# Performance work log

Hardware: AMD Instinct MI355X
Metric: run time of the kernel (lower is better)

The kernel has to match this reference:

```python
import jax, jax.numpy as jnp
import numpy as np

WS = 7          # window_size
NH = 4          # num_heads
C = 128         # channels
N = WS * WS     # tokens per window = 49
BW = 4096       # number of windows total (batch * windows_per_image)
NW = 64         # windows per image (mask leading dim)


def _rel_pos_index(ws):
    coords = np.stack(np.meshgrid(np.arange(ws), np.arange(ws), indexing='ij'))
    cf = coords.reshape(2, -1)
    rel = (cf[:, :, None] - cf[:, None, :]).transpose(1, 2, 0)
    rel[:, :, 0] += ws - 1
    rel[:, :, 1] += ws - 1
    rel[:, :, 0] *= 2 * ws - 1
    return jnp.asarray(rel.sum(-1).ravel(), dtype=jnp.int32)  # [N*N]


def setup_inputs() -> dict:
    key = jax.random.key(0)
    ks = jax.random.split(key, 6)
    x = jax.random.normal(ks[0], (BW, N, C), dtype=jnp.float32)
    qkv_w = jax.random.normal(ks[1], (C, 3 * C), dtype=jnp.float32) * 0.02
    qkv_b = jnp.zeros((3 * C,), dtype=jnp.float32)
    proj_w = jax.random.normal(ks[2], (C, C), dtype=jnp.float32) * 0.02
    proj_b = jnp.zeros((C,), dtype=jnp.float32)
    bias_table = jax.random.normal(ks[3], ((2 * WS - 1) ** 2, NH), dtype=jnp.float32) * 0.02
    # Swin shifted-window mask: 0 where attention allowed, -100 where blocked
    keep = jax.random.bernoulli(ks[4], 0.5, (NW, N, N))
    mask = jnp.where(keep, 0.0, -100.0).astype(jnp.float32)
    return {"x": x, "qkv_w": qkv_w, "qkv_b": qkv_b, "proj_w": proj_w,
            "proj_b": proj_b, "bias_table": bias_table, "mask": mask}


def reference(x, qkv_w, qkv_b, proj_w, proj_b, bias_table, mask):
    B_, n, c = x.shape
    h = NH
    d = c // h
    scale = d ** -0.5

    qkv = x @ qkv_w + qkv_b                       # [B_, N, 3C]
    qkv = qkv.reshape(B_, n, 3, h, d).transpose(2, 0, 3, 1, 4)  # [3, B_, h, N, d]
    q, k, v = qkv[0], qkv[1], qkv[2]

    attn = jnp.einsum('bhnd,bhmd->bhnm', q * scale, k)          # [B_, h, N, N]

    idx = _rel_pos_index(WS)
    rpb = bias_table[idx].reshape(n, n, h).transpose(2, 0, 1)   # [h, N, N]
    attn = attn + rpb[None]

    nW = mask.shape[0]
    attn = attn.reshape(-1, nW, h, n, n) + mask[None, :, None]  # [B, nW, h, N, N]
    attn = attn.reshape(-1, h, n, n)
    attn = jax.nn.softmax(attn, axis=-1)

    out = jnp.einsum('bhnm,bhmd->bhnd', attn, v)  # [B_, h, N, d]
    out = out.transpose(0, 2, 1, 3).reshape(B_, n, c)
    return out @ proj_w + proj_b
```

## Files before the change

### kernel.cpp

```cpp
#include <hip/hip_runtime.h>

#define NTOK 49
#define CH   128
#define NHEAD 4
#define SCALE 0.17677669529663687f

typedef __bf16 bf16x8 __attribute__((ext_vector_type(8)));
typedef short  s16x8  __attribute__((ext_vector_type(8)));
typedef float  f32x4  __attribute__((ext_vector_type(4)));

__device__ __forceinline__ unsigned short f2bf(float f) {
  unsigned int u = __builtin_bit_cast(unsigned int, f);
  u += 0x7FFFu + ((u >> 16) & 1u);
  return (unsigned short)(u >> 16);
}

__device__ __forceinline__ f32x4 mfma_bf16(s16x8 a, s16x8 b, f32x4 c) {
  return __builtin_amdgcn_mfma_f32_16x16x32_bf16(
      __builtin_bit_cast(bf16x8, a), __builtin_bit_cast(bf16x8, b), c, 0, 0, 0);
}

__global__ void prep_kernel(const float* __restrict__ qkv_w,
                            const float* __restrict__ proj_w,
                            const float* __restrict__ bias_table,
                            unsigned short* __restrict__ wT,
                            unsigned short* __restrict__ pT,
                            float* __restrict__ rpb) {
  int t = blockIdx.x * 256 + threadIdx.x;
  if (t < 384 * 128) {
    int n = t >> 7, k = t & 127;
    float v = qkv_w[k * 384 + n];
    if (n < 128) v *= SCALE;
    wT[n * 128 + k] = f2bf(v);
  } else if (t < 384 * 128 + 128 * 128) {
    int u = t - 384 * 128;
    int n = u >> 7, k = u & 127;
    pT[n * 128 + k] = f2bf(proj_w[k * 128 + n]);
  } else if (t < 384 * 128 + 128 * 128 + NHEAD * NTOK * NTOK) {
    int u = t - (384 * 128 + 128 * 128);
    int h = u / (NTOK * NTOK);
    int ij = u % (NTOK * NTOK);
    int i = ij / NTOK, j = ij % NTOK;
    int idx = (i / 7 - j / 7 + 6) * 13 + (i % 7 - j % 7 + 6);
    rpb[h * (NTOK * NTOK) + ij] = bias_table[idx * NHEAD + h];
  }
}

__global__ __launch_bounds__(256, 2)
void attn_fused_kernel(const float* __restrict__ x,
                       const float* __restrict__ qkv_b,
                       const float* __restrict__ proj_b,
                       const float* __restrict__ mask,
                       const unsigned short* __restrict__ wT,
                       const unsigned short* __restrict__ pT,
                       const float* __restrict__ rpb,
                       float* __restrict__ out) {
  __shared__ __align__(16) char smem_raw[76800];
  unsigned short* const Xs     = (unsigned short*)smem_raw;
  unsigned short* const QKbase = (unsigned short*)(smem_raw + 17408);
  unsigned short* const VTbase = (unsigned short*)(smem_raw + 58368);

  const int w    = blockIdx.x;
  const int tid  = threadIdx.x;
  const int wave = tid >> 6;
  const int lane = tid & 63;
  const int quad = lane >> 4;
  const int l16  = lane & 15;
  const int h    = wave;

  unsigned short* const qs = QKbase + wave * 5120;
  unsigned short* const ks = qs + 2560;
  unsigned short* const ps = QKbase + wave * 5120;
  unsigned short* const vt = VTbase + wave * 2304;

  const f32x4 fzero = {0.f, 0.f, 0.f, 0.f};

  {
    const float* xw = x + (size_t)w * (NTOK * CH);
    for (int t = tid; t < NTOK * 32; t += 256) {
      const int row = t >> 5;
      const int c4  = (t & 31) << 2;
      const float4 v = *(const float4*)(xw + row * CH + c4);
      ushort4 pk;
      pk.x = f2bf(v.x); pk.y = f2bf(v.y); pk.z = f2bf(v.z); pk.w = f2bf(v.w);
      *(ushort4*)(Xs + row * 136 + c4) = pk;
    }
    for (int t = tid; t < 15 * 32; t += 256) {
      const int row = 49 + (t >> 5);
      const int c4  = (t & 31) << 2;
      ushort4 z; z.x = 0; z.y = 0; z.z = 0; z.w = 0;
      *(ushort4*)(Xs + row * 136 + c4) = z;
    }
  }
  __syncthreads();

#pragma unroll
  for (int part = 0; part < 3; ++part) {
    f32x4 acc[4][2];
#pragma unroll
    for (int mt = 0; mt < 4; ++mt)
#pragma unroll
      for (int nt = 0; nt < 2; ++nt) acc[mt][nt] = fzero;
    const int nbase = part * 128 + h * 32;
#pragma unroll
    for (int kt = 0; kt < 4; ++kt) {
      s16x8 a[4], b[2];
#pragma unroll
      for (int mt = 0; mt < 4; ++mt)
        a[mt] = *(const s16x8*)(Xs + (mt * 16 + l16) * 136 + kt * 32 + quad * 8);
#pragma unroll
      for (int nt = 0; nt < 2; ++nt)
        b[nt] = *(const s16x8*)(wT + (size_t)(nbase + nt * 16 + l16) * 128 + kt * 32 + quad * 8);
#pragma unroll
      for (int mt = 0; mt < 4; ++mt)
#pragma unroll
        for (int nt = 0; nt < 2; ++nt)
          acc[mt][nt] = mfma_bf16(a[mt], b[nt], acc[mt][nt]);
    }
#pragma unroll
    for (int nt = 0; nt < 2; ++nt) {
      float bias = qkv_b[nbase + nt * 16 + l16];
      if (part == 0) bias *= SCALE;
#pragma unroll
      for (int mt = 0; mt < 4; ++mt)
#pragma unroll
        for (int r = 0; r < 4; ++r) {
          const int row = mt * 16 + quad * 4 + r;
          const int col = nt * 16 + l16;
          const unsigned short bv = f2bf(acc[mt][nt][r] + bias);
          if (part == 0)      qs[row * 40 + col] = bv;
          else if (part == 1) ks[row * 40 + col] = bv;
          else                vt[col * 72 + row] = bv;
        }
    }
  }
  __syncthreads();

  s16x8 qf[4], kf[4];
#pragma unroll
  for (int mt = 0; mt < 4; ++mt)
    qf[mt] = *(const s16x8*)(qs + (mt * 16 + l16) * 40 + quad * 8);
#pragma unroll
  for (int nt = 0; nt < 4; ++nt)
    kf[nt] = *(const s16x8*)(ks + (nt * 16 + l16) * 40 + quad * 8);
  f32x4 s[4][4];
#pragma unroll
  for (int mt = 0; mt < 4; ++mt)
#pragma unroll
    for (int nt = 0; nt < 4; ++nt)
      s[mt][nt] = mfma_bf16(qf[mt], kf[nt], fzero);

  const float* maskw = mask + (size_t)(w & 63) * (NTOK * NTOK);
  const float* rpbh  = rpb + h * (NTOK * NTOK);
  float rinv[4][4];
#pragma unroll
  for (int mt = 0; mt < 4; ++mt) {
#pragma unroll
    for (int r = 0; r < 4; ++r) {
      const int i = mt * 16 + quad * 4 + r;
      float vals[4];
      float vmax = -1e30f;
#pragma unroll
      for (int nt = 0; nt < 4; ++nt) {
        const int j = nt * 16 + l16;
        float v = -1e30f;
        if (i < NTOK && j < NTOK) {
          const int ij = i * NTOK + j;
          v = s[mt][nt][r] + rpbh[ij] + maskw[ij];
        }
        vals[nt] = v;
        vmax = fmaxf(vmax, v);
      }
#pragma unroll
      for (int off = 1; off < 16; off <<= 1)
        vmax = fmaxf(vmax, __shfl_xor(vmax, off, 64));
      float rsum = 0.f;
#pragma unroll
      for (int nt = 0; nt < 4; ++nt) {
        const float e = __expf(vals[nt] - vmax);
        vals[nt] = e;
        rsum += e;
      }
#pragma unroll
      for (int off = 1; off < 16; off <<= 1)
        rsum += __shfl_xor(rsum, off, 64);
      rinv[mt][r] = 1.f / rsum;
#pragma unroll
      for (int nt = 0; nt < 4; ++nt)
        ps[i * 72 + nt * 16 + l16] = f2bf(vals[nt]);
    }
  }

  f32x4 o[4][2];
#pragma unroll
  for (int mt = 0; mt < 4; ++mt)
#pragma unroll
    for (int nt = 0; nt < 2; ++nt) o[mt][nt] = fzero;
#pragma unroll
  for (int kt = 0; kt < 2; ++kt) {
    s16x8 pf[4], vf[2];
#pragma unroll
    for (int mt = 0; mt < 4; ++mt)
      pf[mt] = *(const s16x8*)(ps + (mt * 16 + l16) * 72 + kt * 32 + quad * 8);
#pragma unroll
    for (int nt = 0; nt < 2; ++nt)
      vf[nt] = *(const s16x8*)(vt + (nt * 16 + l16) * 72 + kt * 32 + quad * 8);
#pragma unroll
    for (int mt = 0; mt < 4; ++mt)
#pragma unroll
      for (int nt = 0; nt < 2; ++nt)
        o[mt][nt] = mfma_bf16(pf[mt], vf[nt], o[mt][nt]);
  }

  unsigned short* const ao = Xs;
#pragma unroll
  for (int mt = 0; mt < 4; ++mt)
#pragma unroll
    for (int nt = 0; nt < 2; ++nt)
#pragma unroll
      for (int r = 0; r < 4; ++r) {
        const int row = mt * 16 + quad * 4 + r;
        const int col = h * 32 + nt * 16 + l16;
        ao[row * 136 + col] = f2bf(o[mt][nt][r] * rinv[mt][r]);
      }
  __syncthreads();

  f32x4 po[4][2];
#pragma unroll
  for (int mt = 0; mt < 4; ++mt)
#pragma unroll
    for (int nt = 0; nt < 2; ++nt) po[mt][nt] = fzero;
#pragma unroll
  for (int kt = 0; kt < 4; ++kt) {
    s16x8 a[4], b[2];
#pragma unroll
    for (int mt = 0; mt < 4; ++mt)
      a[mt] = *(const s16x8*)(ao + (mt * 16 + l16) * 136 + kt * 32 + quad * 8);
#pragma unroll
    for (int nt = 0; nt < 2; ++nt)
      b[nt] = *(const s16x8*)(pT + (size_t)(h * 32 + nt * 16 + l16) * 128 + kt * 32 + quad * 8);
#pragma unroll
    for (int mt = 0; mt < 4; ++mt)
#pragma unroll
      for (int nt = 0; nt < 2; ++nt)
        po[mt][nt] = mfma_bf16(a[mt], b[nt], po[mt][nt]);
  }
  float* outw = out + (size_t)w * (NTOK * CH);
#pragma unroll
  for (int nt = 0; nt < 2; ++nt) {
    const int col = h * 32 + nt * 16 + l16;
    const float pb = proj_b[col];
#pragma unroll
    for (int mt = 0; mt < 4; ++mt)
#pragma unroll
      for (int r = 0; r < 4; ++r) {
        const int row = mt * 16 + quad * 4 + r;
        if (row < NTOK) outw[row * CH + col] = po[mt][nt][r] + pb;
      }
  }
}

extern "C" void kernel_launch(void* const* d_in, const int* in_sizes, int n_in,
                              void* d_out, int out_size, void* d_ws, size_t ws_size,
                              hipStream_t stream) {
  (void)in_sizes; (void)n_in; (void)out_size; (void)ws_size;
  const float* x          = (const float*)d_in[0];
  const float* qkv_w      = (const float*)d_in[1];
  const float* qkv_b      = (const float*)d_in[2];
  const float* proj_w     = (const float*)d_in[3];
  const float* proj_b     = (const float*)d_in[4];
  const float* bias_table = (const float*)d_in[5];
  const float* mask       = (const float*)d_in[6];
  float* out = (float*)d_out;

  unsigned short* wT = (unsigned short*)d_ws;
  unsigned short* pT = wT + 384 * 128;
  float* rpb = (float*)(pT + 128 * 128);

  const int prep_items = 384 * 128 + 128 * 128 + NHEAD * NTOK * NTOK;
  prep_kernel<<<(prep_items + 255) / 256, 256, 0, stream>>>(qkv_w, proj_w, bias_table,
                                                            wT, pT, rpb);
  attn_fused_kernel<<<4096, 256, 0, stream>>>(x, qkv_b, proj_b, mask, wT, pT, rpb, out);
}
```

Before: 318.6 us.

## Shrink LDS footprint to fit three blocks per CU via per-wave buffer reuse

Cuts shared memory from 76.8KB to about 54KB by dropping the zero-padded X rows (clamping row indices instead), aliasing the per-wave Q/K, P and V^T buffers, and storing P in two 32-column halves, with the upper half held in registers between the two PV MFMA passes. Launch bounds are raised to 3 blocks per CU to raise occupancy. Q and K projections are fused into one loop, and the block-wide barrier after QKV is removed because each wave only touches its own private region. The price is more register pressure, extra LDS round trips for P, and reliance on inline waitcnt and memory-clobber asm for correctness.

New measurement: 323.1 us. Within noise of the previous version (+1.4%).

```diff
diff --git a/kernel.cpp b/kernel.cpp
--- a/kernel.cpp
+++ b/kernel.cpp
@@ -8,6 +8,8 @@
 typedef __bf16 bf16x8 __attribute__((ext_vector_type(8)));
 typedef short  s16x8  __attribute__((ext_vector_type(8)));
 typedef float  f32x4  __attribute__((ext_vector_type(4)));
+typedef s16x8 s16x8_a __attribute__((may_alias));
+typedef unsigned short u16_a __attribute__((may_alias));
 
 __device__ __forceinline__ unsigned short f2bf(float f) {
   unsigned int u = __builtin_bit_cast(unsigned int, f);
@@ -46,7 +48,7 @@
   }
 }
 
-__global__ __launch_bounds__(256, 2)
+__global__ __launch_bounds__(256, 3)
 void attn_fused_kernel(const float* __restrict__ x,
                        const float* __restrict__ qkv_b,
                        const float* __restrict__ proj_b,
@@ -55,10 +57,8 @@
                        const unsigned short* __restrict__ pT,
                        const float* __restrict__ rpb,
                        float* __restrict__ out) {
-  __shared__ __align__(16) char smem_raw[76800];
-  unsigned short* const Xs     = (unsigned short*)smem_raw;
-  unsigned short* const QKbase = (unsigned short*)(smem_raw + 17408);
-  unsigned short* const VTbase = (unsigned short*)(smem_raw + 58368);
+  __shared__ __align__(16) char smem_raw[54288];
+  unsigned short* const smem = (unsigned short*)smem_raw;
 
   const int w    = blockIdx.x;
   const int tid  = threadIdx.x;
@@ -67,11 +67,15 @@
   const int quad = lane >> 4;
   const int l16  = lane & 15;
   const int h    = wave;
-
-  unsigned short* const qs = QKbase + wave * 5120;
-  unsigned short* const ks = qs + 2560;
-  unsigned short* const ps = QKbase + wave * 5120;
-  unsigned short* const vt = VTbase + wave * 2304;
+  const int wq8  = quad * 8;
+
+  unsigned short* const Xs   = smem;
+  unsigned short* const priv = smem + 6664 + wave * 5120;
+  unsigned short* const qs   = priv;
+  unsigned short* const ks   = priv + 2560;
+  unsigned short* const ps   = priv;
+  unsigned short* const vt   = priv + 2560;
+  unsigned short* const ao   = smem;
 
   const f32x4 fzero = {0.f, 0.f, 0.f, 0.f};
 
@@ -85,64 +89,98 @@
       pk.x = f2bf(v.x); pk.y = f2bf(v.y); pk.z = f2bf(v.z); pk.w = f2bf(v.w);
       *(ushort4*)(Xs + row * 136 + c4) = pk;
     }
-    for (int t = tid; t < 15 * 32; t += 256) {
-      const int row = 49 + (t >> 5);
-      const int c4  = (t & 31) << 2;
-      ushort4 z; z.x = 0; z.y = 0; z.z = 0; z.w = 0;
-      *(ushort4*)(Xs + row * 136 + c4) = z;
+  }
+  __syncthreads();
+
+  int xrow[4];
+#pragma unroll
+  for (int mt = 0; mt < 4; ++mt) {
+    const int rr = mt * 16 + l16;
+    xrow[mt] = (rr < NTOK ? rr : NTOK - 1) * 136;
+  }
+
+  f32x4 accq[4][2], acck[4][2];
+#pragma unroll
+  for (int mt = 0; mt < 4; ++mt)
+#pragma unroll
+    for (int nt = 0; nt < 2; ++nt) { accq[mt][nt] = fzero; acck[mt][nt] = fzero; }
+#pragma unroll
+  for (int kt = 0; kt < 4; ++kt) {
+    s16x8 a[4], bq[2], bk[2];
+#pragma unroll
+    for (int mt = 0; mt < 4; ++mt)
+      a[mt] = *(const s16x8*)(Xs + xrow[mt] + kt * 32 + wq8);
+#pragma unroll
+    for (int nt = 0; nt < 2; ++nt) {
+      const int rowq = h * 32 + nt * 16 + l16;
+      bq[nt] = *(const s16x8*)(wT + (size_t)rowq * 128 + kt * 32 + wq8);
+      bk[nt] = *(const s16x8*)(wT + (size_t)(128 + rowq) * 128 + kt * 32 + wq8);
     }
-  }
-  __syncthreads();
-
-#pragma unroll
-  for (int part = 0; part < 3; ++part) {
-    f32x4 acc[4][2];
-#pragma unroll
-    for (int mt = 0; mt < 4; ++mt)
-#pragma unroll
-      for (int nt = 0; nt < 2; ++nt) acc[mt][nt] = fzero;
-    const int nbase = part * 128 + h * 32;
-#pragma unroll
-    for (int kt = 0; kt < 4; ++kt) {
-      s16x8 a[4], b[2];
-#pragma unroll
-      for (int mt = 0; mt < 4; ++mt)
-        a[mt] = *(const s16x8*)(Xs + (mt * 16 + l16) * 136 + kt * 32 + quad * 8);
+#pragma unroll
+    for (int mt = 0; mt < 4; ++mt)
+#pragma unroll
+      for (int nt = 0; nt < 2; ++nt) {
+        accq[mt][nt] = mfma_bf16(a[mt], bq[nt], accq[mt][nt]);
+        acck[mt][nt] = mfma_bf16(a[mt], bk[nt], acck[mt][nt]);
+      }
+  }
+#pragma unroll
+  for (int nt = 0; nt < 2; ++nt) {
+    const int col = nt * 16 + l16;
+    const float bq_ = qkv_b[h * 32 + col] * SCALE;
+    const float bk_ = qkv_b[128 + h * 32 + col];
+#pragma unroll
+    for (int mt = 0; mt < 4; ++mt)
+#pragma unroll
+      for (int r = 0; r < 4; ++r) {
+        const int row = mt * 16 + quad * 4 + r;
+        *(u16_a*)(qs + row * 40 + col) = f2bf(accq[mt][nt][r] + bq_);
+        *(u16_a*)(ks + row * 40 + col) = f2bf(acck[mt][nt][r] + bk_);
+      }
+  }
+
+  f32x4 accv[4][2];
+#pragma unroll
+  for (int mt = 0; mt < 4; ++mt)
+#pragma unroll
+    for (int nt = 0; nt < 2; ++nt) accv[mt][nt] = fzero;
+#pragma unroll
+  for (int kt = 0; kt < 4; ++kt) {
+    s16x8 a[4], bv[2];
+#pragma unroll
+    for (int mt = 0; mt < 4; ++mt)
+      a[mt] = *(const s16x8*)(Xs + xrow[mt] + kt * 32 + wq8);
+#pragma unroll
+    for (int nt = 0; nt < 2; ++nt)
+      bv[nt] = *(const s16x8*)(wT + (size_t)(256 + h * 32 + nt * 16 + l16) * 128 + kt * 32 + wq8);
+#pragma unroll
+    for (int mt = 0; mt < 4; ++mt)
 #pragma unroll
       for (int nt = 0; nt < 2; ++nt)
-        b[nt] = *(const s16x8*)(wT + (size_t)(nbase + nt * 16 + l16) * 128 + kt * 32 + quad * 8);
-#pragma unroll
-      for (int mt = 0; mt < 4; ++mt)
-#pragma unroll
-        for (int nt = 0; nt < 2; ++nt)
-          acc[mt][nt] = mfma_bf16(a[mt], b[nt], acc[mt][nt]);
-    }
-#pragma unroll
-    for (int nt = 0; nt < 2; ++nt) {
-      float bias = qkv_b[nbase + nt * 16 + l16];
-      if (part == 0) bias *= SCALE;
-#pragma unroll
-      for (int mt = 0; mt < 4; ++mt)
-#pragma unroll
-        for (int r = 0; r < 4; ++r) {
-          const int row = mt * 16 + quad * 4 + r;
-          const int col = nt * 16 + l16;
-          const unsigned short bv = f2bf(acc[mt][nt][r] + bias);
-          if (part == 0)      qs[row * 40 + col] = bv;
-          else if (part == 1) ks[row * 40 + col] = bv;
-          else                vt[col * 72 + row] = bv;
-        }
-    }
-  }
-  __syncthreads();
+        accv[mt][nt] = mfma_bf16(a[mt], bv[nt], accv[mt][nt]);
+  }
 
   s16x8 qf[4], kf[4];
 #pragma unroll
-  for (int mt = 0; mt < 4; ++mt)
-    qf[mt] = *(const s16x8*)(qs + (mt * 16 + l16) * 40 + quad * 8);
-#pragma unroll
-  for (int nt = 0; nt < 4; ++nt)
-    kf[nt] = *(const s16x8*)(ks + (nt * 16 + l16) * 40 + quad * 8);
+  for (int t4 = 0; t4 < 4; ++t4) {
+    qf[t4] = *(const s16x8_a*)(qs + (t4 * 16 + l16) * 40 + wq8);
+    kf[t4] = *(const s16x8_a*)(ks + (t4 * 16 + l16) * 40 + wq8);
+  }
+  asm volatile("s_waitcnt lgkmcnt(0)" ::: "memory");
+
+#pragma unroll
+  for (int nt = 0; nt < 2; ++nt) {
+    const float bv_ = qkv_b[256 + h * 32 + nt * 16 + l16];
+#pragma unroll
+    for (int mt = 0; mt < 4; ++mt)
+#pragma unroll
+      for (int r = 0; r < 4; ++r) {
+        const int row = mt * 16 + quad * 4 + r;
+        const int col = nt * 16 + l16;
+        *(u16_a*)(vt + col * 72 + row) = f2bf(accv[mt][nt][r] + bv_);
+      }
+  }
+
   f32x4 s[4][4];
 #pragma unroll
   for (int mt = 0; mt < 4; ++mt)
@@ -153,6 +191,7 @@
   const float* maskw = mask + (size_t)(w & 63) * (NTOK * NTOK);
   const float* rpbh  = rpb + h * (NTOK * NTOK);
   float rinv[4][4];
+  unsigned int pHold[4][4];
 #pragma unroll
   for (int mt = 0; mt < 4; ++mt) {
 #pragma unroll
@@ -185,9 +224,9 @@
       for (int off = 1; off < 16; off <<= 1)
         rsum += __shfl_xor(rsum, off, 64);
       rinv[mt][r] = 1.f / rsum;
-#pragma unroll
-      for (int nt = 0; nt < 4; ++nt)
-        ps[i * 72 + nt * 16 + l16] = f2bf(vals[nt]);
+      *(u16_a*)(ps + i * 40 + l16)      = f2bf(vals[0]);
+      *(u16_a*)(ps + i * 40 + 16 + l16) = f2bf(vals[1]);
+      pHold[mt][r] = (unsigned int)f2bf(vals[2]) | ((unsigned int)f2bf(vals[3]) << 16);
     }
   }
 
@@ -196,23 +235,46 @@
   for (int mt = 0; mt < 4; ++mt)
 #pragma unroll
     for (int nt = 0; nt < 2; ++nt) o[mt][nt] = fzero;
-#pragma unroll
-  for (int kt = 0; kt < 2; ++kt) {
+  {
     s16x8 pf[4], vf[2];
 #pragma unroll
     for (int mt = 0; mt < 4; ++mt)
-      pf[mt] = *(const s16x8*)(ps + (mt * 16 + l16) * 72 + kt * 32 + quad * 8);
-#pragma unroll
-    for (int nt = 0; nt < 2; ++nt)
-      vf[nt] = *(const s16x8*)(vt + (nt * 16 + l16) * 72 + kt * 32 + quad * 8);
+      pf[mt] = *(const s16x8_a*)(ps + (mt * 16 + l16) * 40 + wq8);
+#pragma unroll
+    for (int nt = 0; nt < 2; ++nt)
+      vf[nt] = *(const s16x8_a*)(vt + (nt * 16 + l16) * 72 + wq8);
 #pragma unroll
     for (int mt = 0; mt < 4; ++mt)
 #pragma unroll
       for (int nt = 0; nt < 2; ++nt)
         o[mt][nt] = mfma_bf16(pf[mt], vf[nt], o[mt][nt]);
   }
-
-  unsigned short* const ao = Xs;
+  asm volatile("" ::: "memory");
+#pragma unroll
+  for (int mt = 0; mt < 4; ++mt)
+#pragma unroll
+    for (int r = 0; r < 4; ++r) {
+      const int i = mt * 16 + quad * 4 + r;
+      *(u16_a*)(ps + i * 40 + l16)      = (unsigned short)(pHold[mt][r] & 0xFFFFu);
+      *(u16_a*)(ps + i * 40 + 16 + l16) = (unsigned short)(pHold[mt][r] >> 16);
+    }
+  asm volatile("" ::: "memory");
+  {
+    s16x8 pf[4], vf[2];
+#pragma unroll
+    for (int mt = 0; mt < 4; ++mt)
+      pf[mt] = *(const s16x8_a*)(ps + (mt * 16 + l16) * 40 + wq8);
+#pragma unroll
+    for (int nt = 0; nt < 2; ++nt)
+      vf[nt] = *(const s16x8_a*)(vt + (nt * 16 + l16) * 72 + 32 + wq8);
+#pragma unroll
+    for (int mt = 0; mt < 4; ++mt)
+#pragma unroll
+      for (int nt = 0; nt < 2; ++nt)
+        o[mt][nt] = mfma_bf16(pf[mt], vf[nt], o[mt][nt]);
+  }
+
+  __syncthreads();
 #pragma unroll
   for (int mt = 0; mt < 4; ++mt)
 #pragma unroll
@@ -220,8 +282,7 @@
 #pragma unroll
       for (int r = 0; r < 4; ++r) {
         const int row = mt * 16 + quad * 4 + r;
-        const int col = h * 32 + nt * 16 + l16;
-        ao[row * 136 + col] = f2bf(o[mt][nt][r] * rinv[mt][r]);
+        *(u16_a*)(ao + row * 136 + h * 32 + nt * 16 + l16) = f2bf(o[mt][nt][r] * rinv[mt][r]);
       }
   __syncthreads();
 
@@ -235,10 +296,10 @@
     s16x8 a[4], b[2];
 #pragma unroll
     for (int mt = 0; mt < 4; ++mt)
-      a[mt] = *(const s16x8*)(ao + (mt * 16 + l16) * 136 + kt * 32 + quad * 8);
-#pragma unroll
-    for (int nt = 0; nt < 2; ++nt)
-      b[nt] = *(const s16x8*)(pT + (size_t)(h * 32 + nt * 16 + l16) * 128 + kt * 32 + quad * 8);
+      a[mt] = *(const s16x8_a*)(ao + (mt * 16 + l16) * 136 + kt * 32 + wq8);
+#pragma unroll
+    for (int nt = 0; nt < 2; ++nt)
+      b[nt] = *(const s16x8*)(pT + (size_t)(h * 32 + nt * 16 + l16) * 128 + kt * 32 + wq8);
 #pragma unroll
     for (int mt = 0; mt < 4; ++mt)
 #pragma unroll
```
